# Kernel tuning notes

Measured on AMD Instinct MI355X. Metric: run time of the kernel, lower is better.

The kernel has to match this reference:

```python
import jax, jax.numpy as jnp
import numpy as np

# dims
B, N, T, D = 32, 207, 12, 128
H, HD, L, FF = 8, 16, 4, 512
PL, OD, IN = 12, 1, 1
SCALE = 1.0 / float(np.sqrt(HD))
NEG = -1e9


def ln(x, g, b, eps=1e-5):
    m = jnp.mean(x, -1, keepdims=True)
    v = jnp.mean((x - m) ** 2, -1, keepdims=True)
    return (x - m) * jax.lax.rsqrt(v + eps) * g + b


def setup_inputs() -> dict:
    key = jax.random.key(0)
    keys = iter(jax.random.split(key, 48))
    def rn(shape, s=0.02):
        return jax.random.normal(next(keys), shape, jnp.float32) * s
    z = lambda *s: jnp.zeros(s, jnp.float32)
    o = lambda *s: jnp.ones(s, jnp.float32)
    inp = {
        "x": jax.random.normal(next(keys), (B, N, T, IN), jnp.float32),
        "adj": jax.random.randint(next(keys), (N, N), 0, 2, jnp.int32),
        "Wi": rn((IN, D)), "bi": z(D),
        # spatial blocks (stacked over L layers)
        "Wq": rn((L, D, D)), "Wk": rn((L, D, D)), "Wv": rn((L, D, D)),
        "Wo": rn((L, D, D)), "bo": z(L, D),
        "sW1": rn((L, D, FF)), "sB1": z(L, FF), "sW2": rn((L, FF, D)), "sB2": z(L, D),
        "sg1": o(L, D), "sh1": z(L, D), "sg2": o(L, D), "sh2": z(L, D),
        # temporal blocks
        "Win": rn((L, D, 3 * D)), "Bin": z(L, 3 * D), "Wout": rn((L, D, D)), "Bout": z(L, D),
        "tW1": rn((L, D, FF)), "tB1": z(L, FF), "tW2": rn((L, FF, D)), "tB2": z(L, D),
        "tg1": o(L, D), "th1": z(L, D), "tg2": o(L, D), "th2": z(L, D),
        # prediction head
        "P1": rn((D, 2 * D)), "Pb1": z(2 * D), "P2": rn((2 * D, D)), "Pb2": z(D),
        "P3": rn((D, PL * OD)), "Pb3": z(PL * OD),
    }
    return inp


def reference(x, adj, Wi, bi, Wq, Wk, Wv, Wo, bo, sW1, sB1, sW2, sB2,
              sg1, sh1, sg2, sh2, Win, Bin, Wout, Bout, tW1, tB1, tW2, tB2,
              tg1, th1, tg2, th2, P1, Pb1, P2, Pb2, P3, Pb3):
    mask = (adj == 0)  # [N,N] True = masked (no edge)
    cmask = jnp.triu(jnp.ones((T, T), bool), 1)  # causal mask over time
    h = x @ Wi + bi  # [B,N,T,D]
    for l in range(L):
        # --- spatial adjacency-masked attention (vectorized over t) ---
        xn = ln(h, sg1[l], sh1[l])
        q = (xn @ Wq[l]).reshape(B, N, T, H, HD)
        k = (xn @ Wk[l]).reshape(B, N, T, H, HD)
        v = (xn @ Wv[l]).reshape(B, N, T, H, HD)
        sc = jnp.einsum('bnthd,bmthd->bthnm', q, k) * SCALE  # [B,T,H,N,N]
        sc = jnp.where(mask[None, None, None], NEG, sc)
        a = jax.nn.softmax(sc, -1)
        o = jnp.einsum('bthnm,bmthd->bnthd', a, v).reshape(B, N, T, D)
        h = h + o @ Wo[l] + bo[l]
        xn = ln(h, sg2[l], sh2[l])
        h = h + jax.nn.relu(xn @ sW1[l] + sB1[l]) @ sW2[l] + sB2[l]
        # --- temporal causal attention (per node) ---
        xn = ln(h, tg1[l], th1[l])
        qkv = xn @ Win[l] + Bin[l]
        q, k, v = jnp.split(qkv, 3, -1)
        q = q.reshape(B, N, T, H, HD)
        k = k.reshape(B, N, T, H, HD)
        v = v.reshape(B, N, T, H, HD)
        sc = jnp.einsum('bnthd,bnshd->bnhts', q, k) * SCALE  # [B,N,H,T,T]
        sc = jnp.where(cmask[None, None, None], NEG, sc)
        a = jax.nn.softmax(sc, -1)
        o = jnp.einsum('bnhts,bnshd->bnthd', a, v).reshape(B, N, T, D)
        h = h + o @ Wout[l] + Bout[l]
        xn = ln(h, tg2[l], th2[l])
        h = h + jax.nn.relu(xn @ tW1[l] + tB1[l]) @ tW2[l] + tB2[l]
    # prediction head on last time step
    hl = h[:, :, -1, :]  # [B,N,D]
    zz = jax.nn.relu(hl @ P1 + Pb1)
    zz = jax.nn.relu(zz @ P2 + Pb2)
    return (zz @ P3 + Pb3).reshape(B, N, PL, OD)
```

## Files before the change

kernel.cpp:

```cpp
#include <hip/hip_runtime.h>
#include <hip/hip_bf16.h>

#define B_   32
#define N_   207
#define T_   12
#define D_   128
#define H_   8
#define HD_  16
#define L_   4
#define FF_  512
#define PL_  12
#define TOK  (B_*N_*T_)
#define ROWS2 (B_*N_)
#define SCALE_ 0.25f
#define LOG2E_ 1.4426950408889634f
#define NEG2_ -1.4426950409e9f
#define KVH  232
#define SLAB 3312
#define MSK_N (13*13*256)

typedef __hip_bfloat16 bf16;
typedef unsigned int u32;
typedef __attribute__((ext_vector_type(4))) unsigned int u32x4;
typedef __attribute__((ext_vector_type(8))) short bf16x8;
typedef __attribute__((ext_vector_type(8))) _Float16 f16x8;
typedef __attribute__((ext_vector_type(4))) float f32x4;

__device__ __forceinline__ float b2f(bf16 x){ return __bfloat162float(x); }
__device__ __forceinline__ bf16  f2b(float x){ return __float2bfloat16(x); }

__device__ __forceinline__ void gll16(const bf16* g, bf16* l){
  __builtin_amdgcn_global_load_lds((const __attribute__((address_space(1))) void*)g,
                                   (__attribute__((address_space(3))) void*)l, 16, 0, 0);
}

__global__ void detect_k(const void* x, int* flag){
  __shared__ int cnt[256];
  const unsigned short* u = (const unsigned short*)x;
  int ok = 0;
  for (int i = threadIdx.x; i < 4096; i += 256){
    unsigned int bits = ((unsigned int)u[i]) << 16;
    float f = __uint_as_float(bits);
    float a = fabsf(f);
    if (f == 0.0f || (a > 1e-4f && a < 64.0f)) ok++;
  }
  cnt[threadIdx.x] = ok;
  __syncthreads();
  for (int s = 128; s > 0; s >>= 1){
    if (threadIdx.x < s) cnt[threadIdx.x] += cnt[threadIdx.x + s];
    __syncthreads();
  }
  if (threadIdx.x == 0) *flag = (cnt[0] > 3686) ? 1 : 0;
}

struct FlatArgs {
  const void* src[24];
  long long dst[24];
  int cum[25];
};
__global__ void cvt_flat_k(FlatArgs a, bf16* base, const int* flag, int total){
  int i = blockIdx.x*256 + threadIdx.x;
  if (i >= total) return;
  int j = 0;
  while (i >= a.cum[j+1]) j++;
  int loc = i - a.cum[j];
  float v = (*flag) ? b2f(((const bf16*)a.src[j])[loc]) : ((const float*)a.src[j])[loc];
  base[a.dst[j] + loc] = f2b(v);
}

struct TArgs {
  const void* src[10];
  long long dst[10];
  int K[10], Nc[10], Lstr[10], ro[10];
  float scale[10];
  int cum[11];
};
__global__ void cvt_t_k(TArgs a, bf16* base, const int* flag, int total){
  int i = blockIdx.x*256 + threadIdx.x;
  if (i >= total) return;
  int j = 0;
  while (i >= a.cum[j+1]) j++;
  int loc = i - a.cum[j];
  int KN = a.K[j]*a.Nc[j];
  int l = loc / KN; int rm = loc - l*KN; int k = rm / a.Nc[j]; int n = rm - k*a.Nc[j];
  float v = (*flag) ? b2f(((const bf16*)a.src[j])[loc]) : ((const float*)a.src[j])[loc];
  base[a.dst[j] + (long long)l*a.Lstr[j] + (long long)(a.ro[j]+n)*a.K[j] + k] = f2b(v*a.scale[j]);
}

__global__ void maskc_k(const int* adj, float* maskg){
  int i = blockIdx.x*256 + threadIdx.x;
  if (i >= MSK_N) return;
  int cell = i >> 8;
  int mi = cell / 13, nj = cell - mi*13;
  int rem = i & 255;
  int lane = rem >> 2, r = rem & 3;
  int quad = lane >> 4, cl = lane & 15;
  int row = mi*16 + quad*4 + r; if (row > 206) row = 206;
  int col = nj*16 + cl;
  float v;
  if (col > 206) v = -1e30f;
  else v = adj[row*N_ + col] ? 0.0f : NEG2_;
  maskg[i] = v;
}

__global__ void embed_ln_k(const bf16* x, const bf16* Wi, const bf16* bi,
                           const bf16* g, const bf16* bta, float* h, bf16* xnb){
  int wave = threadIdx.x >> 6, lane = threadIdx.x & 63;
  int tok = blockIdx.x*4 + wave;
  if (tok >= TOK) return;
  float xv = b2f(x[tok]);
  float v0 = xv*b2f(Wi[lane])    + b2f(bi[lane]);
  float v1 = xv*b2f(Wi[lane+64]) + b2f(bi[lane+64]);
  float* hp = h + (size_t)tok*D_;
  hp[lane] = v0; hp[lane+64] = v1;
  float s = v0 + v1;
  for (int off = 32; off >= 1; off >>= 1) s += __shfl_xor(s, off, 64);
  float m = s * (1.0f/128.0f);
  float d0 = v0 - m, d1 = v1 - m;
  float vv = d0*d0 + d1*d1;
  for (int off = 32; off >= 1; off >>= 1) vv += __shfl_xor(vv, off, 64);
  float r = rsqrtf(vv*(1.0f/128.0f) + 1e-5f);
  bf16* op = xnb + (size_t)tok*D_;
  op[lane]    = f2b(d0*r*b2f(g[lane])    + b2f(bta[lane]));
  op[lane+64] = f2b(d1*r*b2f(g[lane+64]) + b2f(bta[lane+64]));
}

__global__ __launch_bounds__(256) void mgemm_k(const bf16* __restrict__ A,
    const bf16* __restrict__ Wt, const bf16* __restrict__ bias,
    bf16* __restrict__ outp, int ldo, int Ktot, int relu){
  __shared__ __align__(16) bf16 As[128*32];
  __shared__ __align__(16) bf16 Bs[128*32];
  int tid = threadIdx.x;
  int rowBase = blockIdx.y * 128, colBase = blockIdx.x * 128;
  int w = tid >> 6, lane = tid & 63, quad = lane >> 4, cl = lane & 15;
  int waveM = w >> 1, waveN = w & 1;
  f32x4 accr[4][4];
  #pragma unroll
  for (int i = 0; i < 4; i++)
    #pragma unroll
    for (int j = 0; j < 4; j++) accr[i][j] = (f32x4){0.f,0.f,0.f,0.f};
  int lr = tid >> 2, kc = tid & 3;
  const bf16* Ap = A  + (size_t)(rowBase + lr)*Ktot + kc*8;
  const bf16* Bp = Wt + (size_t)(colBase + lr)*Ktot + kc*8;
  bf16* AsW = As + tid*8;
  bf16* BsW = Bs + tid*8;
  for (int kk = 0; kk < Ktot; kk += 32){
    __syncthreads();
    gll16(Ap + kk, AsW);
    gll16(Ap + (size_t)64*Ktot + kk, AsW + 64*32);
    gll16(Bp + kk, BsW);
    gll16(Bp + (size_t)64*Ktot + kk, BsW + 64*32);
    __syncthreads();
    bf16x8 af[4], bfr[4];
    #pragma unroll
    for (int mi = 0; mi < 4; mi++)
      af[mi] = *(const bf16x8*)(As + (waveM*64 + mi*16 + cl)*32 + quad*8);
    #pragma unroll
    for (int nj = 0; nj < 4; nj++)
      bfr[nj] = *(const bf16x8*)(Bs + (waveN*64 + nj*16 + cl)*32 + quad*8);
    #pragma unroll
    for (int mi = 0; mi < 4; mi++)
      #pragma unroll
      for (int nj = 0; nj < 4; nj++)
        accr[mi][nj] = __builtin_amdgcn_mfma_f32_16x16x32_bf16(af[mi], bfr[nj], accr[mi][nj], 0,0,0);
  }
  float bv[4];
  #pragma unroll
  for (int nj = 0; nj < 4; nj++)
    bv[nj] = bias ? b2f(bias[colBase + waveN*64 + nj*16 + cl]) : 0.0f;
  #pragma unroll
  for (int mi = 0; mi < 4; mi++){
    int row0 = rowBase + waveM*64 + mi*16 + quad*4;
    #pragma unroll
    for (int nj = 0; nj < 4; nj++){
      int col = colBase + waveN*64 + nj*16 + cl;
      #pragma unroll
      for (int r = 0; r < 4; r++){
        float v = accr[mi][nj][r] + bv[nj];
        if (relu) v = fmaxf(v, 0.0f);
        outp[(size_t)(row0+r)*ldo + col] = f2b(v);
      }
    }
  }
}

__global__ __launch_bounds__(256) void mgemm_qkvT_k(const bf16* __restrict__ A,
    const bf16* __restrict__ Wt, bf16* __restrict__ sQ,
    bf16* __restrict__ sK, bf16* __restrict__ sV){
  __shared__ __align__(16) bf16 As[128*32];
  __shared__ __align__(16) bf16 Bs[128*32];
  const int Ktot = 128;
  int tid = threadIdx.x;
  int rowBase = blockIdx.y * 128, colBase = blockIdx.x * 128;
  int w = tid >> 6, lane = tid & 63, quad = lane >> 4, cl = lane & 15;
  int waveM = w >> 1, waveN = w & 1;
  f32x4 accr[4][4];
  #pragma unroll
  for (int i = 0; i < 4; i++)
    #pragma unroll
    for (int j = 0; j < 4; j++) accr[i][j] = (f32x4){0.f,0.f,0.f,0.f};
  int lr = tid >> 2, kc = tid & 3;
  const bf16* Ap = A  + (size_t)(rowBase + lr)*Ktot + kc*8;
  const bf16* Bp = Wt + (size_t)(colBase + lr)*Ktot + kc*8;
  bf16* AsW = As + tid*8;
  bf16* BsW = Bs + tid*8;
  for (int kk = 0; kk < Ktot; kk += 32){
    __syncthreads();
    gll16(Ap + kk, AsW);
    gll16(Ap + (size_t)64*Ktot + kk, AsW + 64*32);
    gll16(Bp + kk, BsW);
    gll16(Bp + (size_t)64*Ktot + kk, BsW + 64*32);
    __syncthreads();
    bf16x8 af[4], bfr[4];
    #pragma unroll
    for (int mi = 0; mi < 4; mi++)
      af[mi] = *(const bf16x8*)(As + (waveM*64 + mi*16 + cl)*32 + quad*8);
    #pragma unroll
    for (int nj = 0; nj < 4; nj++)
      bfr[nj] = *(const bf16x8*)(Bs + (waveN*64 + nj*16 + cl)*32 + quad*8);
    #pragma unroll
    for (int mi = 0; mi < 4; mi++)
      #pragma unroll
      for (int nj = 0; nj < 4; nj++)
        accr[mi][nj] = __builtin_amdgcn_mfma_f32_16x16x32_bf16(af[mi], bfr[nj], accr[mi][nj], 0,0,0);
  }
  #pragma unroll
  for (int mi = 0; mi < 4; mi++){
    #pragma unroll
    for (int r = 0; r < 4; r++){
      int tok = rowBase + waveM*64 + mi*16 + quad*4 + r;
      int bn = tok / T_; int t = tok - bn*T_;
      int b = bn / N_;  int n = bn - b*N_;
      size_t base = ((size_t)(b*T_ + t)*H_)*SLAB + n*16 + cl;
      #pragma unroll
      for (int nj = 0; nj < 4; nj++){
        int col = colBase + waveN*64 + nj*16;
        int part = col >> 7, hh = (col >> 4) & 7;
        bf16* dst = (part == 0) ? sQ : (part == 1) ? sK : sV;
        dst[base + (size_t)hh*SLAB] = f2b(accr[mi][nj][r]);
      }
    }
  }
}

__global__ __launch_bounds__(256) void mgemm_ln_k(const bf16* __restrict__ A,
    const bf16* __restrict__ Wt, const bf16* __restrict__ bias,
    float* __restrict__ hout, int Ktot,
    const bf16* __restrict__ g, const bf16* __restrict__ bta,
    bf16* __restrict__ xnb){
  __shared__ __align__(16) bf16 As[128*32];
  __shared__ __align__(16) bf16 Bs[128*32];
  __shared__ float red[2][128][2];
  int tid = threadIdx.x;
  int rowBase = blockIdx.y * 128;
  int w = tid >> 6, lane = tid & 63, quad = lane >> 4, cl = lane & 15;
  int waveM = w >> 1, waveN = w & 1;
  f32x4 accr[4][4];
  #pragma unroll
  for (int i = 0; i < 4; i++)
    #pragma unroll
    for (int j = 0; j < 4; j++) accr[i][j] = (f32x4){0.f,0.f,0.f,0.f};
  int lr = tid >> 2, kc = tid & 3;
  const bf16* Ap = A  + (size_t)(rowBase + lr)*Ktot + kc*8;
  const bf16* Bp = Wt + (size_t)lr*Ktot + kc*8;
  bf16* AsW = As + tid*8;
  bf16* BsW = Bs + tid*8;
  for (int kk = 0; kk < Ktot; kk += 32){
    __syncthreads();
    gll16(Ap + kk, AsW);
    gll16(Ap + (size_t)64*Ktot + kk, AsW + 64*32);
    gll16(Bp + kk, BsW);
    gll16(Bp + (size_t)64*Ktot + kk, BsW + 64*32);
    __syncthreads();
    bf16x8 af[4], bfr[4];
    #pragma unroll
    for (int mi = 0; mi < 4; mi++)
      af[mi] = *(const bf16x8*)(As + (waveM*64 + mi*16 + cl)*32 + quad*8);
    #pragma unroll
    for (int nj = 0; nj < 4; nj++)
      bfr[nj] = *(const bf16x8*)(Bs + (waveN*64 + nj*16 + cl)*32 + quad*8);
    #pragma unroll
    for (int mi = 0; mi < 4; mi++)
      #pragma unroll
      for (int nj = 0; nj < 4; nj++)
        accr[mi][nj] = __builtin_amdgcn_mfma_f32_16x16x32_bf16(af[mi], bfr[nj], accr[mi][nj], 0,0,0);
  }
  int colW = waveN*64;
  float bv[4];
  #pragma unroll
  for (int nj = 0; nj < 4; nj++)
    bv[nj] = bias ? b2f(bias[colW + nj*16 + cl]) : 0.0f;
  float hv[4][4][4];
  float psum[4][4], psq[4][4];
  #pragma unroll
  for (int mi = 0; mi < 4; mi++)
    #pragma unroll
    for (int r = 0; r < 4; r++){ psum[mi][r] = 0.f; psq[mi][r] = 0.f; }
  #pragma unroll
  for (int mi = 0; mi < 4; mi++){
    #pragma unroll
    for (int r = 0; r < 4; r++){
      int row = rowBase + waveM*64 + mi*16 + quad*4 + r;
      #pragma unroll
      for (int nj = 0; nj < 4; nj++){
        int col = colW + nj*16 + cl;
        size_t idx = (size_t)row*D_ + col;
        float v = hout[idx] + accr[mi][nj][r] + bv[nj];
        hout[idx] = v;
        hv[mi][nj][r] = v;
        psum[mi][r] += v; psq[mi][r] += v*v;
      }
    }
  }
  if (g){
    #pragma unroll
    for (int off = 1; off <= 8; off <<= 1)
      #pragma unroll
      for (int mi = 0; mi < 4; mi++)
        #pragma unroll
        for (int r = 0; r < 4; r++){
          psum[mi][r] += __shfl_xor(psum[mi][r], off, 64);
          psq[mi][r]  += __shfl_xor(psq[mi][r],  off, 64);
        }
    if (cl == 0){
      #pragma unroll
      for (int mi = 0; mi < 4; mi++)
        #pragma unroll
        for (int r = 0; r < 4; r++){
          int rl = waveM*64 + mi*16 + quad*4 + r;
          red[waveN][rl][0] = psum[mi][r];
          red[waveN][rl][1] = psq[mi][r];
        }
    }
    __syncthreads();
    float gv[4], btv[4];
    #pragma unroll
    for (int nj = 0; nj < 4; nj++){
      int col = colW + nj*16 + cl;
      gv[nj] = b2f(g[col]); btv[nj] = b2f(bta[col]);
    }
    #pragma unroll
    for (int mi = 0; mi < 4; mi++){
      #pragma unroll
      for (int r = 0; r < 4; r++){
        int rl = waveM*64 + mi*16 + quad*4 + r;
        float s = red[0][rl][0] + red[1][rl][0];
        float q = red[0][rl][1] + red[1][rl][1];
        float mean = s*(1.0f/128.0f);
        float var  = q*(1.0f/128.0f) - mean*mean;
        float rstd = rsqrtf(var + 1e-5f);
        int row = rowBase + rl;
        #pragma unroll
        for (int nj = 0; nj < 4; nj++){
          int col = colW + nj*16 + cl;
          xnb[(size_t)row*D_ + col] = f2b((hv[mi][nj][r]-mean)*rstd*gv[nj] + btv[nj]);
        }
      }
    }
  }
}

__global__ __launch_bounds__(256,2) void mffn_ln_k(const bf16* __restrict__ A,
    const bf16* __restrict__ W1t, const bf16* __restrict__ b1,
    const bf16* __restrict__ W2t, const bf16* __restrict__ b2,
    float* __restrict__ hout,
    const bf16* __restrict__ g, const bf16* __restrict__ bta,
    bf16* __restrict__ xnb){
  __shared__ __align__(16) bf16 As[128*136];
  __shared__ __align__(16) bf16 Hs[128*136];
  __shared__ __align__(16) bf16 Bs[128*32];
  __shared__ float red[2][128][2];
  int tid = threadIdx.x;
  int rowBase = blockIdx.x * 128;
  int w = tid >> 6, lane = tid & 63, quad = lane >> 4, cl = lane & 15;
  int waveM = w >> 1, waveN = w & 1;
  for (int i = tid; i < 128*16; i += 256){
    int row = i >> 4, ch = i & 15;
    u32x4 v = *(const u32x4*)(A + (size_t)(rowBase + row)*128 + ch*8);
    *(u32x4*)(As + row*136 + ch*8) = v;
  }
  f32x4 acc2[4][4];
  #pragma unroll
  for (int i = 0; i < 4; i++)
    #pragma unroll
    for (int j = 0; j < 4; j++) acc2[i][j] = (f32x4){0.f,0.f,0.f,0.f};
  int lr = tid >> 2, kc = tid & 3;
  bf16* BsW = Bs + tid*8;
  int aRow0 = waveM*64;
  for (int kt = 0; kt < 4; kt++){
    f32x4 acc1[4][4];
    #pragma unroll
    for (int i = 0; i < 4; i++)
      #pragma unroll
      for (int j = 0; j < 4; j++) acc1[i][j] = (f32x4){0.f,0.f,0.f,0.f};
    for (int ks = 0; ks < 4; ks++){
      __syncthreads();
      gll16(W1t + (size_t)(kt*128 + lr)*128 + ks*32 + kc*8, BsW);
      gll16(W1t + (size_t)(kt*128 + 64 + lr)*128 + ks*32 + kc*8, BsW + 64*32);
      __syncthreads();
      bf16x8 af[4], bfr[4];
      #pragma unroll
      for (int mi = 0; mi < 4; mi++)
        af[mi] = *(const bf16x8*)(As + (aRow0 + mi*16 + cl)*136 + ks*32 + quad*8);
      #pragma unroll
      for (int nj = 0; nj < 4; nj++)
        bfr[nj] = *(const bf16x8*)(Bs + (waveN*64 + nj*16 + cl)*32 + quad*8);
      #pragma unroll
      for (int mi = 0; mi < 4; mi++)
        #pragma unroll
        for (int nj = 0; nj < 4; nj++)
          acc1[mi][nj] = __builtin_amdgcn_mfma_f32_16x16x32_bf16(af[mi], bfr[nj], acc1[mi][nj], 0,0,0);
    }
    float b1v[4];
    #pragma unroll
    for (int nj = 0; nj < 4; nj++)
      b1v[nj] = b2f(b1[kt*128 + waveN*64 + nj*16 + cl]);
    #pragma unroll
    for (int mi = 0; mi < 4; mi++){
      #pragma unroll
      for (int r = 0; r < 4; r++){
        int row = aRow0 + mi*16 + quad*4 + r;
        #pragma unroll
        for (int nj = 0; nj < 4; nj++){
          int col = waveN*64 + nj*16 + cl;
          Hs[row*136 + col] = f2b(fmaxf(acc1[mi][nj][r] + b1v[nj], 0.0f));
        }
      }
    }
    for (int ks = 0; ks < 4; ks++){
      __syncthreads();
      gll16(W2t + (size_t)lr*512 + kt*128 + ks*32 + kc*8, BsW);
      gll16(W2t + (size_t)(64 + lr)*512 + kt*128 + ks*32 + kc*8, BsW + 64*32);
      __syncthreads();
      bf16x8 af[4], bfr[4];
      #pragma unroll
      for (int mi = 0; mi < 4; mi++)
        af[mi] = *(const bf16x8*)(Hs + (aRow0 + mi*16 + cl)*136 + ks*32 + quad*8);
      #pragma unroll
      for (int nj = 0; nj < 4; nj++)
        bfr[nj] = *(const bf16x8*)(Bs + (waveN*64 + nj*16 + cl)*32 + quad*8);
      #pragma unroll
      for (int mi = 0; mi < 4; mi++)
        #pragma unroll
        for (int nj = 0; nj < 4; nj++)
          acc2[mi][nj] = __builtin_amdgcn_mfma_f32_16x16x32_bf16(af[mi], bfr[nj], acc2[mi][nj], 0,0,0);
    }
    __syncthreads();
  }
  int colW = waveN*64;
  float bv[4];
  #pragma unroll
  for (int nj = 0; nj < 4; nj++)
    bv[nj] = b2f(b2[colW + nj*16 + cl]);
  float hv[4][4][4];
  float psum[4][4], psq[4][4];
  #pragma unroll
  for (int mi = 0; mi < 4; mi++)
    #pragma unroll
    for (int r = 0; r < 4; r++){ psum[mi][r] = 0.f; psq[mi][r] = 0.f; }
  #pragma unroll
  for (int mi = 0; mi < 4; mi++){
    #pragma unroll
    for (int r = 0; r < 4; r++){
      int row = rowBase + aRow0 + mi*16 + quad*4 + r;
      #pragma unroll
      for (int nj = 0; nj < 4; nj++){
        int col = colW + nj*16 + cl;
        size_t idx = (size_t)row*D_ + col;
        float v = hout[idx] + acc2[mi][nj][r] + bv[nj];
        hout[idx] = v;
        hv[mi][nj][r] = v;
        psum[mi][r] += v; psq[mi][r] += v*v;
      }
    }
  }
  if (g){
    #pragma unroll
    for (int off = 1; off <= 8; off <<= 1)
      #pragma unroll
      for (int mi = 0; mi < 4; mi++)
        #pragma unroll
        for (int r = 0; r < 4; r++){
          psum[mi][r] += __shfl_xor(psum[mi][r], off, 64);
          psq[mi][r]  += __shfl_xor(psq[mi][r],  off, 64);
        }
    if (cl == 0){
      #pragma unroll
      for (int mi = 0; mi < 4; mi++)
        #pragma unroll
        for (int r = 0; r < 4; r++){
          int rl = aRow0 + mi*16 + quad*4 + r;
          red[waveN][rl][0] = psum[mi][r];
          red[waveN][rl][1] = psq[mi][r];
        }
    }
    __syncthreads();
    float gv[4], btv[4];
    #pragma unroll
    for (int nj = 0; nj < 4; nj++){
      int col = colW + nj*16 + cl;
      gv[nj] = b2f(g[col]); btv[nj] = b2f(bta[col]);
    }
    #pragma unroll
    for (int mi = 0; mi < 4; mi++){
      #pragma unroll
      for (int r = 0; r < 4; r++){
        int rl = aRow0 + mi*16 + quad*4 + r;
        float s = red[0][rl][0] + red[1][rl][0];
        float q = red[0][rl][1] + red[1][rl][1];
        float mean = s*(1.0f/128.0f);
        float var  = q*(1.0f/128.0f) - mean*mean;
        float rstd = rsqrtf(var + 1e-5f);
        int row = rowBase + rl;
        #pragma unroll
        for (int nj = 0; nj < 4; nj++){
          int col = colW + nj*16 + cl;
          xnb[(size_t)row*D_ + col] = f2b((hv[mi][nj][r]-mean)*rstd*gv[nj] + btv[nj]);
        }
      }
    }
  }
}

__global__ __launch_bounds__(256,4) void sattn_k(const bf16* __restrict__ sQ,
    const bf16* __restrict__ sK, const bf16* __restrict__ sV,
    const float* __restrict__ maskg, bf16* __restrict__ ob){
  __shared__ __align__(16) _Float16 Vt[16*KVH];
  __shared__ __align__(16) _Float16 Ps[4*16*KVH];
  int tid = threadIdx.x;
  int bid = blockIdx.x;
  int hh = bid & 7; int bt = bid >> 3; int t = bt % T_; int b = bt / T_;
  const bf16* Kslab = sK + (size_t)bid*SLAB;
  const bf16* Vslab = sV + (size_t)bid*SLAB;
  const bf16* Qslab = sQ + (size_t)bid*SLAB;
  for (int i = tid; i < 16*25; i += 256){ int d = i/25, c = 207 + i%25; Vt[d*KVH + c] = (_Float16)0.0f; }
  for (int i = tid; i < 64*24; i += 256){ int row = i/24, c = 208 + i%24; Ps[row*KVH + c] = (_Float16)0.0f; }
  for (int i = tid; i < SLAB; i += 256){
    int n = i >> 4, d = i & 15;
    Vt[d*KVH + n] = (_Float16)b2f(Vslab[i]);
  }
  __syncthreads();

  int lane = tid & 63, w = tid >> 6, quad = lane >> 4, cl = lane & 15;
  f16x8 ones8;
  #pragma unroll
  for (int j = 0; j < 8; j++) ones8[j] = (_Float16)1.0f;
  int nstripes = (w == 0) ? 4 : 3;
  for (int si = 0; si < nstripes; si++){
    int mi = w + si*4;
    bf16x8 aq = (bf16x8){0,0,0,0,0,0,0,0};
    {
      int n = mi*16 + cl; if (n > N_-1) n = N_-1;
      if (quad < 2) aq = *(const bf16x8*)(Qslab + n*16 + quad*8);
    }
    const float* mrow = maskg + ((size_t)mi*13)*256 + lane*4;
    f32x4 s[13];
    #pragma unroll
    for (int nj = 0; nj < 13; nj++){
      bf16x8 bk = (bf16x8){0,0,0,0,0,0,0,0};
      if (quad < 2){
        int nb = nj*16 + cl; if (nb > N_-1) nb = N_-1;
        bk = *(const bf16x8*)(Kslab + nb*16 + quad*8);
      }
      f32x4 c0 = *(const f32x4*)(mrow + nj*256);
      s[nj] = __builtin_amdgcn_mfma_f32_16x16x32_bf16(aq, bk, c0, 0,0,0);
    }
    int row0 = mi*16 + quad*4;
    _Float16* Pw = Ps + w*16*KVH;
    #pragma unroll
    for (int r = 0; r < 4; r++){
      _Float16* Pr = Pw + (quad*4 + r)*KVH;
      #pragma unroll
      for (int nj = 0; nj < 13; nj++)
        Pr[nj*16 + cl] = (_Float16)exp2f(s[nj][r]);
    }
    __threadfence_block();
    f32x4 o = {0.f,0.f,0.f,0.f};
    f32x4 osum = {0.f,0.f,0.f,0.f};
    #pragma unroll
    for (int kt = 0; kt < 7; kt++){
      f16x8 ap = *(const f16x8*)(Pw + cl*KVH + kt*32 + quad*8);
      f16x8 bv = *(const f16x8*)(Vt + cl*KVH + kt*32 + quad*8);
      o    = __builtin_amdgcn_mfma_f32_16x16x32_f16(ap, bv,    o,    0,0,0);
      osum = __builtin_amdgcn_mfma_f32_16x16x32_f16(ap, ones8, osum, 0,0,0);
    }
    #pragma unroll
    for (int r = 0; r < 4; r++){
      int rg = row0 + r;
      if (rg < N_)
        ob[((size_t)((b*N_ + rg)*T_ + t))*D_ + hh*HD_ + cl] = f2b(o[r]/osum[r]);
    }
    __threadfence_block();
  }
}

__global__ void tattn_k(const bf16* qkv, bf16* ob){
  int bid = blockIdx.x; int b = bid / N_, n = bid % N_;
  __shared__ float qs[T_*D_];
  __shared__ float ks[T_*D_];
  __shared__ float vs[T_*D_];
  size_t rowb = ((size_t)(b*N_+n)*T_)*384;
  const u32* src = (const u32*)(qkv + rowb);
  for (int idx = threadIdx.x; idx < T_*192; idx += 128){
    int tt = idx / 192, cw = idx - tt*192;
    u32 pr = src[tt*192 + cw];
    union { u32 u; bf16 b[2]; } cv; cv.u = pr;
    float v0 = b2f(cv.b[0]), v1 = b2f(cv.b[1]);
    int arr = cw >> 6, cp2 = (cw & 63)*2;
    float* dst = (arr == 0) ? qs : (arr == 1) ? ks : vs;
    dst[tt*128 + cp2] = v0; dst[tt*128 + cp2 + 1] = v1;
  }
  __syncthreads();
  int p = threadIdx.x;
  if (p < H_*T_){
    int hh = p / T_, t = p - hh*T_;
    float qreg[16];
    for (int d = 0; d < 16; d++) qreg[d] = qs[t*128 + hh*16 + d];
    float sc[12]; float mx = -3.4e38f;
    for (int s = 0; s < 12; s++){
      float a = 0.0f;
      for (int d = 0; d < 16; d++) a += qreg[d]*ks[s*128 + hh*16 + d];
      a = (s <= t) ? a*SCALE_ : -3.4e38f;
      sc[s] = a; mx = fmaxf(mx, a);
    }
    float ssum = 0.0f;
    for (int s = 0; s < 12; s++){
      float e = (s <= t) ? __expf(sc[s]-mx) : 0.0f;
      sc[s] = e; ssum += e;
    }
    float inv = 1.0f/ssum;
    size_t obase = ((size_t)(b*N_+n)*T_ + t)*D_ + hh*16;
    for (int d = 0; d < 16; d++){
      float acc = 0.0f;
      for (int s = 0; s < 12; s++) acc += sc[s]*vs[s*128 + hh*16 + d];
      ob[obase + d] = f2b(acc*inv);
    }
  }
}

__global__ void gemm_k(const bf16* A, int lda, const bf16* W, const bf16* bias,
                       void* outp, int ldo, int M, int Ncols, int K, int relu, int acc){
  __shared__ float Ast[16*68];
  __shared__ float Ws [16*68];
  int tx = threadIdx.x & 15, ty = threadIdx.x >> 4;
  int rowBase = blockIdx.y * 64, colBase = blockIdx.x * 64;
  float accr[4][4];
  for (int i = 0; i < 4; i++) for (int j = 0; j < 4; j++) accr[i][j] = 0.0f;
  for (int kk = 0; kk < K; kk += 16){
    int kq = threadIdx.x & 15, r0 = threadIdx.x >> 4;
    for (int it = 0; it < 4; it++){
      int r = r0 + it*16, row = rowBase + r;
      float v = 0.0f;
      if (row < M) v = b2f(A[(size_t)row*lda + kk + kq]);
      Ast[kq*68 + r] = v;
    }
    int c = threadIdx.x & 63, w0 = threadIdx.x >> 6;
    for (int it = 0; it < 4; it++){
      int kr = w0 + it*4;
      Ws[kr*68 + c] = b2f(W[(size_t)(kk+kr)*Ncols + colBase + c]);
    }
    __syncthreads();
    for (int k = 0; k < 16; k++){
      float av[4], wv[4];
      for (int i = 0; i < 4; i++) av[i] = Ast[k*68 + ty*4 + i];
      for (int j = 0; j < 4; j++) wv[j] = Ws[k*68 + tx*4 + j];
      for (int i = 0; i < 4; i++)
        for (int j = 0; j < 4; j++) accr[i][j] += av[i]*wv[j];
    }
    __syncthreads();
  }
  for (int i = 0; i < 4; i++){
    int row = rowBase + ty*4 + i;
    if (row >= M) continue;
    for (int j = 0; j < 4; j++){
      int col = colBase + tx*4 + j;
      float v = accr[i][j];
      if (bias) v += b2f(bias[col]);
      if (relu) v = fmaxf(v, 0.0f);
      if (acc) ((float*)outp)[(size_t)row*ldo + col] += v;
      else     ((bf16*)outp)[(size_t)row*ldo + col] = f2b(v);
    }
  }
}

__global__ void gather_k(const float* h, bf16* hlb){
  int i = blockIdx.x*256 + threadIdx.x;
  if (i >= ROWS2*D_) return;
  int r = i >> 7, d = i & 127;
  hlb[i] = f2b(h[((size_t)r*T_ + (T_-1))*D_ + d]);
}

__global__ void head3_k(const bf16* z2, const bf16* P3, const bf16* Pb3,
                        void* out, int out_n, const int* flag){
  int i = blockIdx.x*256 + threadIdx.x;
  if (i >= out_n) return;
  int r = i / PL_, j = i - r*PL_;
  float acc = b2f(Pb3[j]);
  for (int d = 0; d < 128; d++) acc += b2f(z2[(size_t)r*128 + d]) * b2f(P3[d*PL_ + j]);
  if (*flag) ((bf16*)out)[i] = f2b(acc);
  else       ((float*)out)[i] = acc;
}

extern "C" void kernel_launch(void* const* d_in, const int* in_sizes, int n_in,
                              void* d_out, int out_size, void* d_ws, size_t ws_size,
                              hipStream_t stream){
  size_t HB = (size_t)TOK*D_*4;
  size_t XB = (size_t)TOK*D_*2;
  size_t RB = (size_t)TOK*D_*8;
  float* h    = (float*)d_ws;
  bf16*  xnb  = (bf16*)((char*)d_ws + HB);
  bf16*  reg_ = (bf16*)((char*)d_ws + HB + XB);
  bf16*  cvt  = (bf16*)((char*)d_ws + HB + XB + RB);
  bf16*  wsb  = (bf16*)d_ws;
  const int FIDX[34] = {0,2,3,4,5,6,7,8,9,10,11,12,13,14,15,16,17,18,19,20,
                        21,22,23,24,25,26,27,28,29,30,31,32,33,34};
  bf16* cp[34];
  size_t off = 0;
  for (int i = 0; i < 34; i++){ cp[i] = cvt + off; off += (size_t)in_sizes[FIDX[i]]; }
  char* tail   = (char*)d_ws + HB + XB + RB + ((off*2 + 255) & ~(size_t)255);
  float* maskg = (float*)tail;
  bf16* qkvw   = (bf16*)(tail + (size_t)MSK_N*4);
  int*  flag   = (int*)(tail + (size_t)MSK_N*4 + (size_t)L_*384*128*2);

  const bf16 *x_c=cp[0], *Wi_c=cp[1], *bi_c=cp[2],
             *Wo_t=cp[6], *bo_c=cp[7], *sW1_t=cp[8], *sB1_c=cp[9], *sW2_t=cp[10], *sB2_c=cp[11],
             *sg1_c=cp[12], *sh1_c=cp[13], *sg2_c=cp[14], *sh2_c=cp[15], *Win_t=cp[16], *Bin_c=cp[17],
             *Wout_t=cp[18], *Bout_c=cp[19], *tW1_t=cp[20], *tB1_c=cp[21], *tW2_t=cp[22], *tB2_c=cp[23],
             *tg1_c=cp[24], *th1_c=cp[25], *tg2_c=cp[26], *th2_c=cp[27], *P1_c=cp[28], *Pb1_c=cp[29],
             *P2_c=cp[30], *Pb2_c=cp[31], *P3_c=cp[32], *Pb3_c=cp[33];
  const int* adj = (const int*)d_in[1];

  bf16* sQ   = reg_;
  bf16* sK   = reg_ + (size_t)TOK*128;
  bf16* sV   = reg_ + (size_t)2*TOK*128;
  bf16* ob   = reg_ + (size_t)3*TOK*128;
  bf16* qkvb = reg_;

  detect_k<<<1, 256, 0, stream>>>(d_in[0], flag);

  {
    const int FLAT[24] = {0,1,2,7,9,11,12,13,14,15,17,19,21,23,24,25,26,27,28,29,30,31,32,33};
    FlatArgs fa; int c = 0;
    for (int ii = 0; ii < 24; ii++){
      int ci = FLAT[ii];
      fa.src[ii] = d_in[FIDX[ci]];
      fa.dst[ii] = (long long)(cp[ci] - wsb);
      fa.cum[ii] = c;
      c += in_sizes[FIDX[ci]];
    }
    fa.cum[24] = c;
    cvt_flat_k<<<(c+255)/256, 256, 0, stream>>>(fa, wsb, flag, c);
  }
  {
    TArgs ta; int c = 0;
    const void* srcs[10] = {d_in[4], d_in[5], d_in[6], d_in[7], d_in[9], d_in[11],
                            d_in[17], d_in[19], d_in[21], d_in[23]};
    bf16* dsts[10] = {qkvw, qkvw, qkvw, cp[6], cp[8], cp[10], cp[16], cp[18], cp[20], cp[22]};
    int Ks_[10]   = {128,128,128, 128, 128, 512, 128, 128, 128, 512};
    int Ncs[10]   = {128,128,128, 128, 512, 128, 384, 128, 512, 128};
    int Lst[10]   = {384*128,384*128,384*128, 128*128, 128*512, 512*128, 128*384, 128*128, 128*512, 512*128};
    int ros[10]   = {0,128,256, 0,0,0, 0,0,0, 0};
    for (int j = 0; j < 10; j++){
      ta.src[j] = srcs[j];
      ta.dst[j] = (long long)(dsts[j] - wsb);
      ta.K[j] = Ks_[j]; ta.Nc[j] = Ncs[j]; ta.Lstr[j] = Lst[j]; ta.ro[j] = ros[j];
      ta.scale[j] = (j == 0) ? SCALE_*LOG2E_ : 1.0f;
      ta.cum[j] = c;
      c += L_*Ks_[j]*Ncs[j];
    }
    ta.cum[10] = c;
    cvt_t_k<<<(c+255)/256, 256, 0, stream>>>(ta, wsb, flag, c);
  }
  maskc_k<<<(MSK_N+255)/256, 256, 0, stream>>>(adj, maskg);
  embed_ln_k<<<TOK/4, 256, 0, stream>>>(x_c, Wi_c, bi_c, sg1_c, sh1_c, h, xnb);

  const dim3 gP  (1, TOK/128);
  const dim3 gQKV(3, TOK/128);

  for (int l = 0; l < L_; l++){
    mgemm_qkvT_k<<<gQKV, 256, 0, stream>>>(xnb, qkvw + (size_t)l*384*128, sQ, sK, sV);
    sattn_k<<<B_*T_*H_, 256, 0, stream>>>(sQ, sK, sV, maskg, ob);
    mgemm_ln_k<<<gP, 256, 0, stream>>>(ob, Wo_t + (size_t)l*D_*D_, bo_c + l*D_, h, D_,
                                       sg2_c + l*D_, sh2_c + l*D_, xnb);
    mffn_ln_k<<<TOK/128, 256, 0, stream>>>(xnb, sW1_t + (size_t)l*D_*FF_, sB1_c + l*FF_,
                                           sW2_t + (size_t)l*FF_*D_, sB2_c + l*D_, h,
                                           tg1_c + l*D_, th1_c + l*D_, xnb);
    mgemm_k<<<gQKV, 256, 0, stream>>>(xnb, Win_t + (size_t)l*D_*384, Bin_c + l*384, qkvb, 384, D_, 0);
    tattn_k<<<B_*N_, 128, 0, stream>>>(qkvb, ob);
    mgemm_ln_k<<<gP, 256, 0, stream>>>(ob, Wout_t + (size_t)l*D_*D_, Bout_c + l*D_, h, D_,
                                       tg2_c + l*D_, th2_c + l*D_, xnb);
    const bf16* gnext = (l < L_-1) ? (sg1_c + (l+1)*D_) : nullptr;
    const bf16* bnext = (l < L_-1) ? (sh1_c + (l+1)*D_) : nullptr;
    mffn_ln_k<<<TOK/128, 256, 0, stream>>>(xnb, tW1_t + (size_t)l*D_*FF_, tB1_c + l*FF_,
                                           tW2_t + (size_t)l*FF_*D_, tB2_c + l*D_, h,
                                           gnext, bnext, xnb);
  }

  bf16* hlb = reg_;
  bf16* z1  = reg_ + (size_t)ROWS2*128;
  bf16* z2  = z1   + (size_t)ROWS2*256;
  gather_k<<<(ROWS2*D_)/256, 256, 0, stream>>>(h, hlb);
  gemm_k<<<dim3(256/64, (ROWS2+63)/64), 256, 0, stream>>>(hlb, 128, P1_c, Pb1_c, z1, 256, ROWS2, 256, 128, 1, 0);
  gemm_k<<<dim3(128/64, (ROWS2+63)/64), 256, 0, stream>>>(z1, 256, P2_c, Pb2_c, z2, 128, ROWS2, 128, 256, 1, 0);
  head3_k<<<(out_size+255)/256, 256, 0, stream>>>(z2, P3_c, Pb3_c, d_out, out_size, flag);
}
```

Before: 1.571 ms.

## Fuse attention output projection with LN and FFN into one kernel

Merges the output-projection GEMM plus residual and LayerNorm kernel into the following FFN kernel, for both the spatial and temporal blocks. The normalized activations now stay in shared memory (As) rather than being written to and reread from global xnb, and the intermediate h residual is carried in accumulators instead of being stored and reloaded. This removes two launches per layer and one global round trip of h and xnb, but adds register pressure in a kernel already bounded at 2 blocks per CU.

```diff
diff --git a/kernel.cpp b/kernel.cpp
--- a/kernel.cpp
+++ b/kernel.cpp
@@ -243,128 +243,13 @@
   }
 }
 
-__global__ __launch_bounds__(256) void mgemm_ln_k(const bf16* __restrict__ A,
-    const bf16* __restrict__ Wt, const bf16* __restrict__ bias,
-    float* __restrict__ hout, int Ktot,
-    const bf16* __restrict__ g, const bf16* __restrict__ bta,
-    bf16* __restrict__ xnb){
-  __shared__ __align__(16) bf16 As[128*32];
-  __shared__ __align__(16) bf16 Bs[128*32];
-  __shared__ float red[2][128][2];
-  int tid = threadIdx.x;
-  int rowBase = blockIdx.y * 128;
-  int w = tid >> 6, lane = tid & 63, quad = lane >> 4, cl = lane & 15;
-  int waveM = w >> 1, waveN = w & 1;
-  f32x4 accr[4][4];
-  #pragma unroll
-  for (int i = 0; i < 4; i++)
-    #pragma unroll
-    for (int j = 0; j < 4; j++) accr[i][j] = (f32x4){0.f,0.f,0.f,0.f};
-  int lr = tid >> 2, kc = tid & 3;
-  const bf16* Ap = A  + (size_t)(rowBase + lr)*Ktot + kc*8;
-  const bf16* Bp = Wt + (size_t)lr*Ktot + kc*8;
-  bf16* AsW = As + tid*8;
-  bf16* BsW = Bs + tid*8;
-  for (int kk = 0; kk < Ktot; kk += 32){
-    __syncthreads();
-    gll16(Ap + kk, AsW);
-    gll16(Ap + (size_t)64*Ktot + kk, AsW + 64*32);
-    gll16(Bp + kk, BsW);
-    gll16(Bp + (size_t)64*Ktot + kk, BsW + 64*32);
-    __syncthreads();
-    bf16x8 af[4], bfr[4];
-    #pragma unroll
-    for (int mi = 0; mi < 4; mi++)
-      af[mi] = *(const bf16x8*)(As + (waveM*64 + mi*16 + cl)*32 + quad*8);
-    #pragma unroll
-    for (int nj = 0; nj < 4; nj++)
-      bfr[nj] = *(const bf16x8*)(Bs + (waveN*64 + nj*16 + cl)*32 + quad*8);
-    #pragma unroll
-    for (int mi = 0; mi < 4; mi++)
-      #pragma unroll
-      for (int nj = 0; nj < 4; nj++)
-        accr[mi][nj] = __builtin_amdgcn_mfma_f32_16x16x32_bf16(af[mi], bfr[nj], accr[mi][nj], 0,0,0);
-  }
-  int colW = waveN*64;
-  float bv[4];
-  #pragma unroll
-  for (int nj = 0; nj < 4; nj++)
-    bv[nj] = bias ? b2f(bias[colW + nj*16 + cl]) : 0.0f;
-  float hv[4][4][4];
-  float psum[4][4], psq[4][4];
-  #pragma unroll
-  for (int mi = 0; mi < 4; mi++)
-    #pragma unroll
-    for (int r = 0; r < 4; r++){ psum[mi][r] = 0.f; psq[mi][r] = 0.f; }
-  #pragma unroll
-  for (int mi = 0; mi < 4; mi++){
-    #pragma unroll
-    for (int r = 0; r < 4; r++){
-      int row = rowBase + waveM*64 + mi*16 + quad*4 + r;
-      #pragma unroll
-      for (int nj = 0; nj < 4; nj++){
-        int col = colW + nj*16 + cl;
-        size_t idx = (size_t)row*D_ + col;
-        float v = hout[idx] + accr[mi][nj][r] + bv[nj];
-        hout[idx] = v;
-        hv[mi][nj][r] = v;
-        psum[mi][r] += v; psq[mi][r] += v*v;
-      }
-    }
-  }
-  if (g){
-    #pragma unroll
-    for (int off = 1; off <= 8; off <<= 1)
-      #pragma unroll
-      for (int mi = 0; mi < 4; mi++)
-        #pragma unroll
-        for (int r = 0; r < 4; r++){
-          psum[mi][r] += __shfl_xor(psum[mi][r], off, 64);
-          psq[mi][r]  += __shfl_xor(psq[mi][r],  off, 64);
-        }
-    if (cl == 0){
-      #pragma unroll
-      for (int mi = 0; mi < 4; mi++)
-        #pragma unroll
-        for (int r = 0; r < 4; r++){
-          int rl = waveM*64 + mi*16 + quad*4 + r;
-          red[waveN][rl][0] = psum[mi][r];
-          red[waveN][rl][1] = psq[mi][r];
-        }
-    }
-    __syncthreads();
-    float gv[4], btv[4];
-    #pragma unroll
-    for (int nj = 0; nj < 4; nj++){
-      int col = colW + nj*16 + cl;
-      gv[nj] = b2f(g[col]); btv[nj] = b2f(bta[col]);
-    }
-    #pragma unroll
-    for (int mi = 0; mi < 4; mi++){
-      #pragma unroll
-      for (int r = 0; r < 4; r++){
-        int rl = waveM*64 + mi*16 + quad*4 + r;
-        float s = red[0][rl][0] + red[1][rl][0];
-        float q = red[0][rl][1] + red[1][rl][1];
-        float mean = s*(1.0f/128.0f);
-        float var  = q*(1.0f/128.0f) - mean*mean;
-        float rstd = rsqrtf(var + 1e-5f);
-        int row = rowBase + rl;
-        #pragma unroll
-        for (int nj = 0; nj < 4; nj++){
-          int col = colW + nj*16 + cl;
-          xnb[(size_t)row*D_ + col] = f2b((hv[mi][nj][r]-mean)*rstd*gv[nj] + btv[nj]);
-        }
-      }
-    }
-  }
-}
-
-__global__ __launch_bounds__(256,2) void mffn_ln_k(const bf16* __restrict__ A,
+__global__ __launch_bounds__(256,2) void projffn_ln_k(const bf16* __restrict__ A,
+    const bf16* __restrict__ Wpt, const bf16* __restrict__ bp,
+    const bf16* __restrict__ g1, const bf16* __restrict__ n1,
     const bf16* __restrict__ W1t, const bf16* __restrict__ b1,
     const bf16* __restrict__ W2t, const bf16* __restrict__ b2,
     float* __restrict__ hout,
-    const bf16* __restrict__ g, const bf16* __restrict__ bta,
+    const bf16* __restrict__ g2, const bf16* __restrict__ n2,
     bf16* __restrict__ xnb){
   __shared__ __align__(16) bf16 As[128*136];
   __shared__ __align__(16) bf16 Hs[128*136];
@@ -374,19 +259,109 @@
   int rowBase = blockIdx.x * 128;
   int w = tid >> 6, lane = tid & 63, quad = lane >> 4, cl = lane & 15;
   int waveM = w >> 1, waveN = w & 1;
+  int lr = tid >> 2, kc = tid & 3;
+  bf16* BsW = Bs + tid*8;
+  int aRow0 = waveM*64;
+  int colW = waveN*64;
+
   for (int i = tid; i < 128*16; i += 256){
     int row = i >> 4, ch = i & 15;
     u32x4 v = *(const u32x4*)(A + (size_t)(rowBase + row)*128 + ch*8);
     *(u32x4*)(As + row*136 + ch*8) = v;
   }
-  f32x4 acc2[4][4];
+  f32x4 acc[4][4];
   #pragma unroll
   for (int i = 0; i < 4; i++)
     #pragma unroll
-    for (int j = 0; j < 4; j++) acc2[i][j] = (f32x4){0.f,0.f,0.f,0.f};
-  int lr = tid >> 2, kc = tid & 3;
-  bf16* BsW = Bs + tid*8;
-  int aRow0 = waveM*64;
+    for (int j = 0; j < 4; j++) acc[i][j] = (f32x4){0.f,0.f,0.f,0.f};
+  for (int ks = 0; ks < 4; ks++){
+    __syncthreads();
+    gll16(Wpt + (size_t)lr*128 + ks*32 + kc*8, BsW);
+    gll16(Wpt + (size_t)(64 + lr)*128 + ks*32 + kc*8, BsW + 64*32);
+    __syncthreads();
+    bf16x8 af[4], bfr[4];
+    #pragma unroll
+    for (int mi = 0; mi < 4; mi++)
+      af[mi] = *(const bf16x8*)(As + (aRow0 + mi*16 + cl)*136 + ks*32 + quad*8);
+    #pragma unroll
+    for (int nj = 0; nj < 4; nj++)
+      bfr[nj] = *(const bf16x8*)(Bs + (colW + nj*16 + cl)*32 + quad*8);
+    #pragma unroll
+    for (int mi = 0; mi < 4; mi++)
+      #pragma unroll
+      for (int nj = 0; nj < 4; nj++)
+        acc[mi][nj] = __builtin_amdgcn_mfma_f32_16x16x32_bf16(af[mi], bfr[nj], acc[mi][nj], 0,0,0);
+  }
+  {
+    float bvp[4];
+    #pragma unroll
+    for (int nj = 0; nj < 4; nj++)
+      bvp[nj] = b2f(bp[colW + nj*16 + cl]);
+    float hv[4][4][4];
+    float psum[4][4], psq[4][4];
+    #pragma unroll
+    for (int mi = 0; mi < 4; mi++)
+      #pragma unroll
+      for (int r = 0; r < 4; r++){ psum[mi][r] = 0.f; psq[mi][r] = 0.f; }
+    #pragma unroll
+    for (int mi = 0; mi < 4; mi++){
+      #pragma unroll
+      for (int r = 0; r < 4; r++){
+        int row = rowBase + aRow0 + mi*16 + quad*4 + r;
+        #pragma unroll
+        for (int nj = 0; nj < 4; nj++){
+          acc[mi][nj][r] += bvp[nj];
+          int col = colW + nj*16 + cl;
+          float v = hout[(size_t)row*D_ + col] + acc[mi][nj][r];
+          hv[mi][nj][r] = v;
+          psum[mi][r] += v; psq[mi][r] += v*v;
+        }
+      }
+    }
+    #pragma unroll
+    for (int off = 1; off <= 8; off <<= 1)
+      #pragma unroll
+      for (int mi = 0; mi < 4; mi++)
+        #pragma unroll
+        for (int r = 0; r < 4; r++){
+          psum[mi][r] += __shfl_xor(psum[mi][r], off, 64);
+          psq[mi][r]  += __shfl_xor(psq[mi][r],  off, 64);
+        }
+    if (cl == 0){
+      #pragma unroll
+      for (int mi = 0; mi < 4; mi++)
+        #pragma unroll
+        for (int r = 0; r < 4; r++){
+          int rl = aRow0 + mi*16 + quad*4 + r;
+          red[waveN][rl][0] = psum[mi][r];
+          red[waveN][rl][1] = psq[mi][r];
+        }
+    }
+    __syncthreads();
+    float gv[4], btv[4];
+    #pragma unroll
+    for (int nj = 0; nj < 4; nj++){
+      int col = colW + nj*16 + cl;
+      gv[nj] = b2f(g1[col]); btv[nj] = b2f(n1[col]);
+    }
+    #pragma unroll
+    for (int mi = 0; mi < 4; mi++){
+      #pragma unroll
+      for (int r = 0; r < 4; r++){
+        int rl = aRow0 + mi*16 + quad*4 + r;
+        float s = red[0][rl][0] + red[1][rl][0];
+        float q = red[0][rl][1] + red[1][rl][1];
+        float mean = s*(1.0f/128.0f);
+        float var  = q*(1.0f/128.0f) - mean*mean;
+        float rstd = rsqrtf(var + 1e-5f);
+        #pragma unroll
+        for (int nj = 0; nj < 4; nj++){
+          int col = colW + nj*16 + cl;
+          As[rl*136 + col] = f2b((hv[mi][nj][r]-mean)*rstd*gv[nj] + btv[nj]);
+        }
+      }
+    }
+  }
   for (int kt = 0; kt < 4; kt++){
     f32x4 acc1[4][4];
     #pragma unroll
@@ -404,7 +379,7 @@
         af[mi] = *(const bf16x8*)(As + (aRow0 + mi*16 + cl)*136 + ks*32 + quad*8);
       #pragma unroll
       for (int nj = 0; nj < 4; nj++)
-        bfr[nj] = *(const bf16x8*)(Bs + (waveN*64 + nj*16 + cl)*32 + quad*8);
+        bfr[nj] = *(const bf16x8*)(Bs + (colW + nj*16 + cl)*32 + quad*8);
       #pragma unroll
       for (int mi = 0; mi < 4; mi++)
         #pragma unroll
@@ -414,7 +389,7 @@
     float b1v[4];
     #pragma unroll
     for (int nj = 0; nj < 4; nj++)
-      b1v[nj] = b2f(b1[kt*128 + waveN*64 + nj*16 + cl]);
+      b1v[nj] = b2f(b1[kt*128 + colW + nj*16 + cl]);
     #pragma unroll
     for (int mi = 0; mi < 4; mi++){
       #pragma unroll
@@ -422,7 +397,7 @@
         int row = aRow0 + mi*16 + quad*4 + r;
         #pragma unroll
         for (int nj = 0; nj < 4; nj++){
-          int col = waveN*64 + nj*16 + cl;
+          int col = colW + nj*16 + cl;
           Hs[row*136 + col] = f2b(fmaxf(acc1[mi][nj][r] + b1v[nj], 0.0f));
         }
       }
@@ -438,84 +413,85 @@
         af[mi] = *(const bf16x8*)(Hs + (aRow0 + mi*16 + cl)*136 + ks*32 + quad*8);
       #pragma unroll
       for (int nj = 0; nj < 4; nj++)
-        bfr[nj] = *(const bf16x8*)(Bs + (waveN*64 + nj*16 + cl)*32 + quad*8);
+        bfr[nj] = *(const bf16x8*)(Bs + (colW + nj*16 + cl)*32 + quad*8);
       #pragma unroll
       for (int mi = 0; mi < 4; mi++)
         #pragma unroll
         for (int nj = 0; nj < 4; nj++)
-          acc2[mi][nj] = __builtin_amdgcn_mfma_f32_16x16x32_bf16(af[mi], bfr[nj], acc2[mi][nj], 0,0,0);
-    }
-    __syncthreads();
-  }
-  int colW = waveN*64;
-  float bv[4];
-  #pragma unroll
-  for (int nj = 0; nj < 4; nj++)
-    bv[nj] = b2f(b2[colW + nj*16 + cl]);
-  float hv[4][4][4];
-  float psum[4][4], psq[4][4];
-  #pragma unroll
-  for (int mi = 0; mi < 4; mi++)
-    #pragma unroll
-    for (int r = 0; r < 4; r++){ psum[mi][r] = 0.f; psq[mi][r] = 0.f; }
-  #pragma unroll
-  for (int mi = 0; mi < 4; mi++){
-    #pragma unroll
-    for (int r = 0; r < 4; r++){
-      int row = rowBase + aRow0 + mi*16 + quad*4 + r;
+          acc[mi][nj] = __builtin_amdgcn_mfma_f32_16x16x32_bf16(af[mi], bfr[nj], acc[mi][nj], 0,0,0);
+    }
+    __syncthreads();
+  }
+  {
+    float bv2[4];
+    #pragma unroll
+    for (int nj = 0; nj < 4; nj++)
+      bv2[nj] = b2f(b2[colW + nj*16 + cl]);
+    float hv[4][4][4];
+    float psum[4][4], psq[4][4];
+    #pragma unroll
+    for (int mi = 0; mi < 4; mi++)
+      #pragma unroll
+      for (int r = 0; r < 4; r++){ psum[mi][r] = 0.f; psq[mi][r] = 0.f; }
+    #pragma unroll
+    for (int mi = 0; mi < 4; mi++){
+      #pragma unroll
+      for (int r = 0; r < 4; r++){
+        int row = rowBase + aRow0 + mi*16 + quad*4 + r;
+        #pragma unroll
+        for (int nj = 0; nj < 4; nj++){
+          int col = colW + nj*16 + cl;
+          size_t idx = (size_t)row*D_ + col;
+          float v = hout[idx] + acc[mi][nj][r] + bv2[nj];
+          hout[idx] = v;
+          hv[mi][nj][r] = v;
+          psum[mi][r] += v; psq[mi][r] += v*v;
+        }
+      }
+    }
+    if (g2){
+      #pragma unroll
+      for (int off = 1; off <= 8; off <<= 1)
+        #pragma unroll
+        for (int mi = 0; mi < 4; mi++)
+          #pragma unroll
+          for (int r = 0; r < 4; r++){
+            psum[mi][r] += __shfl_xor(psum[mi][r], off, 64);
+            psq[mi][r]  += __shfl_xor(psq[mi][r],  off, 64);
+          }
+      if (cl == 0){
+        #pragma unroll
+        for (int mi = 0; mi < 4; mi++)
+          #pragma unroll
+          for (int r = 0; r < 4; r++){
+            int rl = aRow0 + mi*16 + quad*4 + r;
+            red[waveN][rl][0] = psum[mi][r];
+            red[waveN][rl][1] = psq[mi][r];
+          }
+      }
+      __syncthreads();
+      float gv[4], btv[4];
       #pragma unroll
       for (int nj = 0; nj < 4; nj++){
         int col = colW + nj*16 + cl;
-        size_t idx = (size_t)row*D_ + col;
-        float v = hout[idx] + acc2[mi][nj][r] + bv[nj];
-        hout[idx] = v;
-        hv[mi][nj][r] = v;
-        psum[mi][r] += v; psq[mi][r] += v*v;
-      }
-    }
-  }
-  if (g){
-    #pragma unroll
-    for (int off = 1; off <= 8; off <<= 1)
-      #pragma unroll
-      for (int mi = 0; mi < 4; mi++)
-        #pragma unroll
-        for (int r = 0; r < 4; r++){
-          psum[mi][r] += __shfl_xor(psum[mi][r], off, 64);
-          psq[mi][r]  += __shfl_xor(psq[mi][r],  off, 64);
-        }
-    if (cl == 0){
-      #pragma unroll
-      for (int mi = 0; mi < 4; mi++)
+        gv[nj] = b2f(g2[col]); btv[nj] = b2f(n2[col]);
+      }
+      #pragma unroll
+      for (int mi = 0; mi < 4; mi++){
         #pragma unroll
         for (int r = 0; r < 4; r++){
           int rl = aRow0 + mi*16 + quad*4 + r;
-          red[waveN][rl][0] = psum[mi][r];
-          red[waveN][rl][1] = psq[mi][r];
-        }
-    }
-    __syncthreads();
-    float gv[4], btv[4];
-    #pragma unroll
-    for (int nj = 0; nj < 4; nj++){
-      int col = colW + nj*16 + cl;
-      gv[nj] = b2f(g[col]); btv[nj] = b2f(bta[col]);
-    }
-    #pragma unroll
-    for (int mi = 0; mi < 4; mi++){
-      #pragma unroll
-      for (int r = 0; r < 4; r++){
-        int rl = aRow0 + mi*16 + quad*4 + r;
-        float s = red[0][rl][0] + red[1][rl][0];
-        float q = red[0][rl][1] + red[1][rl][1];
-        float mean = s*(1.0f/128.0f);
-        float var  = q*(1.0f/128.0f) - mean*mean;
-        float rstd = rsqrtf(var + 1e-5f);
-        int row = rowBase + rl;
-        #pragma unroll
-        for (int nj = 0; nj < 4; nj++){
-          int col = colW + nj*16 + cl;
-          xnb[(size_t)row*D_ + col] = f2b((hv[mi][nj][r]-mean)*rstd*gv[nj] + btv[nj]);
+          float s = red[0][rl][0] + red[1][rl][0];
+          float q = red[0][rl][1] + red[1][rl][1];
+          float mean = s*(1.0f/128.0f);
+          float var  = q*(1.0f/128.0f) - mean*mean;
+          float rstd = rsqrtf(var + 1e-5f);
+          int row = rowBase + rl;
+          #pragma unroll
+          for (int nj = 0; nj < 4; nj++){
+            int col = colW + nj*16 + cl;
+            xnb[(size_t)row*D_ + col] = f2b((hv[mi][nj][r]-mean)*rstd*gv[nj] + btv[nj]);
+          }
         }
       }
     }
@@ -774,26 +750,25 @@
   maskc_k<<<(MSK_N+255)/256, 256, 0, stream>>>(adj, maskg);
   embed_ln_k<<<TOK/4, 256, 0, stream>>>(x_c, Wi_c, bi_c, sg1_c, sh1_c, h, xnb);
 
-  const dim3 gP  (1, TOK/128);
   const dim3 gQKV(3, TOK/128);
 
   for (int l = 0; l < L_; l++){
     mgemm_qkvT_k<<<gQKV, 256, 0, stream>>>(xnb, qkvw + (size_t)l*384*128, sQ, sK, sV);
     sattn_k<<<B_*T_*H_, 256, 0, stream>>>(sQ, sK, sV, maskg, ob);
-    mgemm_ln_k<<<gP, 256, 0, stream>>>(ob, Wo_t + (size_t)l*D_*D_, bo_c + l*D_, h, D_,
-                                       sg2_c + l*D_, sh2_c + l*D_, xnb);
-    mffn_ln_k<<<TOK/128, 256, 0, stream>>>(xnb, sW1_t + (size_t)l*D_*FF_, sB1_c + l*FF_,
-                                           sW2_t + (size_t)l*FF_*D_, sB2_c + l*D_, h,
-                                           tg1_c + l*D_, th1_c + l*D_, xnb);
+    projffn_ln_k<<<TOK/128, 256, 0, stream>>>(ob, Wo_t + (size_t)l*D_*D_, bo_c + l*D_,
+        sg2_c + l*D_, sh2_c + l*D_,
+        sW1_t + (size_t)l*D_*FF_, sB1_c + l*FF_,
+        sW2_t + (size_t)l*FF_*D_, sB2_c + l*D_, h,
+        tg1_c + l*D_, th1_c + l*D_, xnb);
     mgemm_k<<<gQKV, 256, 0, stream>>>(xnb, Win_t + (size_t)l*D_*384, Bin_c + l*384, qkvb, 384, D_, 0);
     tattn_k<<<B_*N_, 128, 0, stream>>>(qkvb, ob);
-    mgemm_ln_k<<<gP, 256, 0, stream>>>(ob, Wout_t + (size_t)l*D_*D_, Bout_c + l*D_, h, D_,
-                                       tg2_c + l*D_, th2_c + l*D_, xnb);
     const bf16* gnext = (l < L_-1) ? (sg1_c + (l+1)*D_) : nullptr;
     const bf16* bnext = (l < L_-1) ? (sh1_c + (l+1)*D_) : nullptr;
-    mffn_ln_k<<<TOK/128, 256, 0, stream>>>(xnb, tW1_t + (size_t)l*D_*FF_, tB1_c + l*FF_,
-                                           tW2_t + (size_t)l*FF_*D_, tB2_c + l*D_, h,
-                                           gnext, bnext, xnb);
+    projffn_ln_k<<<TOK/128, 256, 0, stream>>>(ob, Wout_t + (size_t)l*D_*D_, Bout_c + l*D_,
+        tg2_c + l*D_, th2_c + l*D_,
+        tW1_t + (size_t)l*D_*FF_, tB1_c + l*FF_,
+        tW2_t + (size_t)l*FF_*D_, tB2_c + l*D_, h,
+        gnext, bnext, xnb);
   }
 
   bf16* hlb = reg_;
```

Result: slower. 1.648 ms (+4.9%).
